# Kernel optimization log

Measured on AMD Instinct MI355X. Metric: run time of the kernel, lower is better.

The kernel has to match this reference:

```python
import jax, jax.numpy as jnp
import numpy as np

N_HEADS = 16

def setup_inputs() -> dict:
    key = jax.random.key(0)
    ks = jax.random.split(key, 6)
    B, S, D = 2, 2048, 1024
    return {
        "hidden_states": jax.random.normal(ks[0], (B, S, D), dtype=jnp.float32),
        "Wq": jax.random.normal(ks[1], (D, D), dtype=jnp.float32) * (1.0 / np.sqrt(D)),
        "Wk": jax.random.normal(ks[2], (D, D), dtype=jnp.float32) * (1.0 / np.sqrt(D)),
        "Wv": jax.random.normal(ks[3], (D, D), dtype=jnp.float32) * (1.0 / np.sqrt(D)),
        "Wo": jax.random.normal(ks[4], (D, D), dtype=jnp.float32) * (1.0 / np.sqrt(D)),
        "bo": jnp.zeros((D,), dtype=jnp.float32),
    }

def reference(hidden_states, Wq, Wk, Wv, Wo, bo):
    B, S, D = hidden_states.shape
    H = N_HEADS
    hd = D // H  # head_dim; d_kv == d_model per module's final view
    # nn.Linear(bias=False): x @ W.T, then the module's direct view to (B, H, S, hd)
    q = (hidden_states @ Wq.T).reshape(B, H, S, hd)
    k = (hidden_states @ Wk.T).reshape(B, H, S, hd)  # self-attention path (encoder_states=None)
    v = (hidden_states @ Wv.T).reshape(B, H, S, hd)
    # naive full score matrix [B, H, S, S]
    wei = jnp.einsum('bhqd,bhkd->bhqk', q, k)
    causal = jnp.tril(jnp.ones((S, S), dtype=bool))
    wei = jnp.where(causal, wei, -jnp.inf)
    # NOTE: module divides logits by head_dim (not sqrt) -- preserved faithfully
    attn = jax.nn.softmax(wei / hd, axis=-1)
    ctx = jnp.einsum('bhqk,bhkd->bhqd', attn, v)  # [B, H, S, hd]
    out = ctx.transpose(0, 2, 1, 3).reshape(B, S, D)
    return out @ Wo.T + bo
```

## Files before the change

### kernel.cpp

```cpp
#include <hip/hip_runtime.h>

#define S_LEN   2048
#define D_MODEL 1024
#define N_HEADS 16
#define HEAD_DIM 64

typedef unsigned short u16;
typedef float  floatx4 __attribute__((ext_vector_type(4)));
typedef short  bf16x8  __attribute__((ext_vector_type(8)));

__device__ __forceinline__ u16 f2bf(float f) {
    unsigned int u = __float_as_uint(f);
    u += 0x7FFF + ((u >> 16) & 1);
    return (u16)(u >> 16);
}
__device__ __forceinline__ unsigned pack2bf(float a, float b) {
    return (unsigned)f2bf(a) | ((unsigned)f2bf(b) << 16);
}

__device__ __forceinline__ void gload_lds16(const void* g, void* l) {
    __builtin_amdgcn_global_load_lds(
        reinterpret_cast<const __attribute__((address_space(1))) unsigned int*>(
            reinterpret_cast<uintptr_t>(g)),
        reinterpret_cast<__attribute__((address_space(3))) unsigned int*>(
            reinterpret_cast<uintptr_t>(l)),
        16, 0, 0);
}

__global__ __launch_bounds__(256) void cast_hs(const float* __restrict__ src,
                                               u16* __restrict__ dst) {
    const int i = (blockIdx.x * 256 + threadIdx.x) * 8;
    const float4 a = *(const float4*)(src + i);
    const float4 b = *(const float4*)(src + i + 4);
    uint4 o;
    o.x = pack2bf(a.x, a.y); o.y = pack2bf(a.z, a.w);
    o.z = pack2bf(b.x, b.y); o.w = pack2bf(b.z, b.w);
    *(uint4*)(dst + i) = o;
}

__global__ __launch_bounds__(256) void cast_w(const float* __restrict__ w0,
                                              const float* __restrict__ w1,
                                              const float* __restrict__ w2,
                                              const float* __restrict__ w3,
                                              u16* __restrict__ dst) {
    const float* srcs[4] = {w0, w1, w2, w3};
    const float* src = srcs[blockIdx.y];
    u16* o = dst + (size_t)blockIdx.y * (D_MODEL * D_MODEL);
    const int i = (blockIdx.x * 256 + threadIdx.x) * 8;
    const float4 a = *(const float4*)(src + i);
    const float4 b = *(const float4*)(src + i + 4);
    uint4 v;
    v.x = pack2bf(a.x, a.y); v.y = pack2bf(a.z, a.w);
    v.z = pack2bf(b.x, b.y); v.w = pack2bf(b.z, b.w);
    *(uint4*)(o + i) = v;
}

__global__ __launch_bounds__(256) void vtrans(const u16* __restrict__ Vf,
                                              u16* __restrict__ Vt) {
    __shared__ unsigned T[64 * 133];
    const int bh = blockIdx.y;
    const int sBase = blockIdx.x * 128;
    const u16* src = Vf + (size_t)bh * (S_LEN * HEAD_DIM) + (size_t)sBase * HEAD_DIM;
    u16* dst = Vt + (size_t)bh * (S_LEN * HEAD_DIM) + sBase;
    const int tid = threadIdx.x;

#pragma unroll
    for (int it = 0; it < 4; ++it) {
        const int idx = it * 256 + tid;
        const int row = idx >> 3, ch = idx & 7;
        const float4 v4 = *(const float4*)(src + row * 64 + ch * 8);
        const u16* vs = (const u16*)&v4;
#pragma unroll
        for (int j = 0; j < 8; ++j) T[(ch * 8 + j) * 133 + row] = vs[j];
    }
    __syncthreads();
#pragma unroll
    for (int it = 0; it < 4; ++it) {
        const int idx = it * 256 + tid;
        const int d = idx >> 4, sc = idx & 15;
        union { u16 u[8]; float4 f; } tmp;
#pragma unroll
        for (int j = 0; j < 8; ++j) tmp.u[j] = (u16)T[d * 133 + sc * 8 + j];
        *(float4*)(dst + (size_t)d * S_LEN + sc * 8) = tmp.f;
    }
}

__global__ __launch_bounds__(256) void gemm_qkv(const u16* __restrict__ A,
                                                const u16* __restrict__ Wq,
                                                const u16* __restrict__ Wk,
                                                const u16* __restrict__ Wv,
                                                u16* __restrict__ Qo,
                                                u16* __restrict__ Ko,
                                                u16* __restrict__ Vfo) {
    __shared__ u16 As[8 * 512];
    __shared__ u16 Ws[8 * 512];

    const int which = blockIdx.x >> 3;
    const int nBase = (blockIdx.x & 7) * 128;
    const int mBase = blockIdx.y * 128;
    const u16* W = which == 0 ? Wq : which == 1 ? Wk : Wv;

    const int tid = threadIdx.x, lane = tid & 63, wv = tid >> 6;
    const int l15 = lane & 15, quad = lane >> 4;
    const int wm = wv & 1, wn = wv >> 1;
    const int srow = lane >> 2;
    const int gch  = (lane & 3) ^ ((lane >> 3) & 3);
    const int swz  = (l15 >> 1) & 3;

    floatx4 acc[4][4];
#pragma unroll
    for (int i = 0; i < 4; ++i)
#pragma unroll
        for (int j = 0; j < 4; ++j) acc[i][j] = (floatx4)(0.0f);

    for (int k0 = 0; k0 < D_MODEL; k0 += 32) {
        __syncthreads();
#pragma unroll
        for (int t = 0; t < 2; ++t) {
            const int ci = wv * 2 + t;
            gload_lds16(A + (size_t)(mBase + ci * 16 + srow) * D_MODEL + k0 + gch * 8,
                        &As[ci * 512]);
            gload_lds16(W + (size_t)(nBase + ci * 16 + srow) * D_MODEL + k0 + gch * 8,
                        &Ws[ci * 512]);
        }
        __syncthreads();

        bf16x8 af[4], bfr[4];
#pragma unroll
        for (int mt = 0; mt < 4; ++mt)
            af[mt] = *(const bf16x8*)&As[(wm * 64 + mt * 16 + l15) * 32 + (quad ^ swz) * 8];
#pragma unroll
        for (int nt = 0; nt < 4; ++nt)
            bfr[nt] = *(const bf16x8*)&Ws[(wn * 64 + nt * 16 + l15) * 32 + (quad ^ swz) * 8];
#pragma unroll
        for (int mt = 0; mt < 4; ++mt)
#pragma unroll
            for (int nt = 0; nt < 4; ++nt)
                acc[mt][nt] = __builtin_amdgcn_mfma_f32_16x16x32_bf16(af[mt], bfr[nt], acc[mt][nt], 0, 0, 0);
    }

    u16* O = which == 0 ? Qo : (which == 1 ? Ko : Vfo);
    const float scale = which == 0 ? (1.44269504088896f / 64.0f) : 1.0f;
#pragma unroll
    for (int mt = 0; mt < 4; ++mt)
#pragma unroll
        for (int nt = 0; nt < 4; ++nt) {
            const int col = nBase + wn * 64 + nt * 16 + l15;
#pragma unroll
            for (int r = 0; r < 4; ++r) {
                const int row = mBase + wm * 64 + mt * 16 + quad * 4 + r;
                O[(size_t)row * D_MODEL + col] = f2bf(acc[mt][nt][r] * scale);
            }
        }
}

__global__ __launch_bounds__(256) void gemm_out(const u16* __restrict__ A,
                                                const u16* __restrict__ W,
                                                const float* __restrict__ bias,
                                                float* __restrict__ C) {
    __shared__ u16 As[8 * 512];
    __shared__ u16 Ws[8 * 512];

    const int nBase = blockIdx.x * 128;
    const int mBase = blockIdx.y * 128;
    const int tid = threadIdx.x, lane = tid & 63, wv = tid >> 6;
    const int l15 = lane & 15, quad = lane >> 4;
    const int wm = wv & 1, wn = wv >> 1;
    const int srow = lane >> 2;
    const int gch  = (lane & 3) ^ ((lane >> 3) & 3);
    const int swz  = (l15 >> 1) & 3;

    floatx4 acc[4][4];
#pragma unroll
    for (int i = 0; i < 4; ++i)
#pragma unroll
        for (int j = 0; j < 4; ++j) acc[i][j] = (floatx4)(0.0f);

    for (int k0 = 0; k0 < D_MODEL; k0 += 32) {
        __syncthreads();
#pragma unroll
        for (int t = 0; t < 2; ++t) {
            const int ci = wv * 2 + t;
            gload_lds16(A + (size_t)(mBase + ci * 16 + srow) * D_MODEL + k0 + gch * 8,
                        &As[ci * 512]);
            gload_lds16(W + (size_t)(nBase + ci * 16 + srow) * D_MODEL + k0 + gch * 8,
                        &Ws[ci * 512]);
        }
        __syncthreads();

        bf16x8 af[4], bfr[4];
#pragma unroll
        for (int mt = 0; mt < 4; ++mt)
            af[mt] = *(const bf16x8*)&As[(wm * 64 + mt * 16 + l15) * 32 + (quad ^ swz) * 8];
#pragma unroll
        for (int nt = 0; nt < 4; ++nt)
            bfr[nt] = *(const bf16x8*)&Ws[(wn * 64 + nt * 16 + l15) * 32 + (quad ^ swz) * 8];
#pragma unroll
        for (int mt = 0; mt < 4; ++mt)
#pragma unroll
            for (int nt = 0; nt < 4; ++nt)
                acc[mt][nt] = __builtin_amdgcn_mfma_f32_16x16x32_bf16(af[mt], bfr[nt], acc[mt][nt], 0, 0, 0);
    }

#pragma unroll
    for (int mt = 0; mt < 4; ++mt)
#pragma unroll
        for (int nt = 0; nt < 4; ++nt) {
            const int col = nBase + wn * 64 + nt * 16 + l15;
            const float bv = bias[col];
#pragma unroll
            for (int r = 0; r < 4; ++r) {
                const int row = mBase + wm * 64 + mt * 16 + quad * 4 + r;
                C[(size_t)row * D_MODEL + col] = acc[mt][nt][r] + bv;
            }
        }
}

__global__ __launch_bounds__(256) void attn2(const u16* __restrict__ Q,
                                             const u16* __restrict__ K,
                                             const u16* __restrict__ Vt,
                                             u16* __restrict__ Ctx) {
    __shared__ u16 Ks[8 * 512];
    __shared__ u16 Vs[8 * 512];
    __shared__ u16 Ps[4][16 * 72];

    const int pair = blockIdx.x;
    const int h = blockIdx.y, b = blockIdx.z;
    const int tid = threadIdx.x, lane = tid & 63, wv = tid >> 6;
    const int l15 = lane & 15, quad = lane >> 4;

    const size_t headOff = ((size_t)b * N_HEADS + h) * S_LEN * HEAD_DIM;
    const u16* Qh = Q + headOff;
    const u16* Kh = K + headOff;
    const u16* Vh = Vt + headOff;
    u16* Cb = Ctx + (size_t)b * S_LEN * D_MODEL + (size_t)h * HEAD_DIM;

    const int srow = lane >> 3;
    const int gch  = (lane & 7) ^ srow;
    const int swz  = l15 & 7;

    for (int half = 0; half < 2; ++half) {
        const int qt = half ? (31 - pair) : pair;
        const int qBase = qt * 64;

        bf16x8 qa[2];
#pragma unroll
        for (int ks = 0; ks < 2; ++ks)
            qa[ks] = *(const bf16x8*)(Qh + (size_t)(qBase + wv * 16 + l15) * 64 + ks * 32 + quad * 8);

        floatx4 o[4];
        float lp[4];
#pragma unroll
        for (int r = 0; r < 4; ++r) lp[r] = 0.0f;
#pragma unroll
        for (int nt = 0; nt < 4; ++nt) o[nt] = (floatx4)(0.0f);

        for (int kt = 0; kt <= qt; ++kt) {
            const int kBase = kt * 64;
            __syncthreads();
#pragma unroll
            for (int t = 0; t < 2; ++t) {
                const int ci = wv * 2 + t;
                gload_lds16(Kh + (size_t)(kBase + ci * 8 + srow) * 64 + gch * 8, &Ks[ci * 512]);
                gload_lds16(Vh + (size_t)(ci * 8 + srow) * S_LEN + kBase + gch * 8, &Vs[ci * 512]);
            }
            __syncthreads();

            floatx4 s[4];
#pragma unroll
            for (int nt = 0; nt < 4; ++nt) {
                s[nt] = (floatx4)(0.0f);
#pragma unroll
                for (int ks = 0; ks < 2; ++ks) {
                    const bf16x8 kb = *(const bf16x8*)&Ks[(nt * 16 + l15) * 64 + ((ks * 4 + quad) ^ swz) * 8];
                    s[nt] = __builtin_amdgcn_mfma_f32_16x16x32_bf16(qa[ks], kb, s[nt], 0, 0, 0);
                }
            }

            if (kt == qt) {
                const int dq = kBase + l15 - (qBase + wv * 16 + quad * 4);
#pragma unroll
                for (int nt = 0; nt < 4; ++nt)
#pragma unroll
                    for (int r = 0; r < 4; ++r) {
                        float p = exp2f(s[nt][r]);
                        p = (dq + nt * 16 > r) ? 0.0f : p;
                        lp[r] += p;
                        Ps[wv][(quad * 4 + r) * 72 + nt * 16 + l15] =
                            (u16)(__float_as_uint(p) >> 16);
                    }
            } else {
#pragma unroll
                for (int nt = 0; nt < 4; ++nt)
#pragma unroll
                    for (int r = 0; r < 4; ++r) {
                        const float p = exp2f(s[nt][r]);
                        lp[r] += p;
                        Ps[wv][(quad * 4 + r) * 72 + nt * 16 + l15] =
                            (u16)(__float_as_uint(p) >> 16);
                    }
            }

            bf16x8 pa[2];
#pragma unroll
            for (int ks = 0; ks < 2; ++ks)
                pa[ks] = *(const bf16x8*)&Ps[wv][l15 * 72 + ks * 32 + quad * 8];
#pragma unroll
            for (int nt = 0; nt < 4; ++nt)
#pragma unroll
                for (int ks = 0; ks < 2; ++ks) {
                    const bf16x8 vb = *(const bf16x8*)&Vs[(nt * 16 + l15) * 64 + ((ks * 4 + quad) ^ swz) * 8];
                    o[nt] = __builtin_amdgcn_mfma_f32_16x16x32_bf16(pa[ks], vb, o[nt], 0, 0, 0);
                }
        }

#pragma unroll
        for (int r = 0; r < 4; ++r) {
#pragma unroll
            for (int off = 1; off < 16; off <<= 1) lp[r] += __shfl_xor(lp[r], off);
            const float inv = 1.0f / lp[r];
            const int row = qBase + wv * 16 + quad * 4 + r;
#pragma unroll
            for (int nt = 0; nt < 4; ++nt)
                Cb[(size_t)row * D_MODEL + nt * 16 + l15] = f2bf(o[nt][r] * inv);
        }
    }
}

extern "C" void kernel_launch(void* const* d_in, const int* in_sizes, int n_in,
                              void* d_out, int out_size, void* d_ws, size_t ws_size,
                              hipStream_t stream) {
    const float* hs = (const float*)d_in[0];
    const float* Wq = (const float*)d_in[1];
    const float* Wk = (const float*)d_in[2];
    const float* Wv = (const float*)d_in[3];
    const float* Wo = (const float*)d_in[4];
    const float* bo = (const float*)d_in[5];
    float* out = (float*)d_out;

    const size_t NHS = (size_t)2 * S_LEN * D_MODEL;
    const size_t NW  = (size_t)D_MODEL * D_MODEL;

    u16* hsb = (u16*)d_ws;
    u16* Wb  = hsb + NHS;
    u16* Qb  = Wb + 4 * NW;
    u16* Kb  = Qb + NHS;
    u16* Vfb = Kb + NHS;
    u16* Vtb = Vfb + NHS;
    u16* Cxb = Vtb + NHS;

    cast_hs<<<2048, 256, 0, stream>>>(hs, hsb);
    cast_w<<<dim3(512, 4), 256, 0, stream>>>(Wq, Wk, Wv, Wo, Wb);

    gemm_qkv<<<dim3(24, 32), 256, 0, stream>>>(hsb, Wb, Wb + NW, Wb + 2 * NW,
                                               Qb, Kb, Vfb);

    vtrans<<<dim3(16, 32), 256, 0, stream>>>(Vfb, Vtb);

    attn2<<<dim3(16, N_HEADS, 2), 256, 0, stream>>>(Qb, Kb, Vtb, Cxb);

    gemm_out<<<dim3(8, 32), 256, 0, stream>>>(Cxb, Wb + 3 * NW, bo, out);
}
```

Baseline: 198.0 us.

## Double-buffer attention K/V loads, transpose score MFMA, merge casts, shrink out-GEMM tile

The attention kernel now double-buffers the K and V tiles in LDS, so the next tile's global-to-LDS load is issued while the current tile is being computed, and each iteration needs one barrier instead of two. It also swaps the MFMA operands so each lane holds a column of scores, which allows packed 64-bit stores of P and a single row-sum reduction, and it remaps the block index so blocks of the same head land near each other. The two cast kernels are merged into one launch, and the output GEMM uses 64-row tiles to double its grid for better occupancy across CUs. The cost is more LDS per attention block and less data reuse per output-GEMM block.

New measurement: 178.4 us. 1.11x faster.

```diff
diff --git a/kernel.cpp b/kernel.cpp
--- a/kernel.cpp
+++ b/kernel.cpp
@@ -27,32 +27,29 @@
         16, 0, 0);
 }
 
-__global__ __launch_bounds__(256) void cast_hs(const float* __restrict__ src,
-                                               u16* __restrict__ dst) {
-    const int i = (blockIdx.x * 256 + threadIdx.x) * 8;
-    const float4 a = *(const float4*)(src + i);
-    const float4 b = *(const float4*)(src + i + 4);
+__global__ __launch_bounds__(256) void cast_all(const float* __restrict__ hs,
+                                                const float* __restrict__ w0,
+                                                const float* __restrict__ w1,
+                                                const float* __restrict__ w2,
+                                                const float* __restrict__ w3,
+                                                u16* __restrict__ dst) {
+    const size_t NHS = (size_t)2 * S_LEN * D_MODEL;
+    const size_t e0 = (size_t)blockIdx.x * 2048;
+    const float* src;
+    size_t base;
+    if (e0 < NHS)                 { src = hs; base = 0; }
+    else {
+        const int wi = (int)((e0 - NHS) >> 20);
+        src = wi == 0 ? w0 : wi == 1 ? w1 : wi == 2 ? w2 : w3;
+        base = NHS + ((size_t)wi << 20);
+    }
+    const size_t i = e0 + (size_t)threadIdx.x * 8;
+    const float4 a = *(const float4*)(src + (i - base));
+    const float4 b = *(const float4*)(src + (i - base) + 4);
     uint4 o;
     o.x = pack2bf(a.x, a.y); o.y = pack2bf(a.z, a.w);
     o.z = pack2bf(b.x, b.y); o.w = pack2bf(b.z, b.w);
     *(uint4*)(dst + i) = o;
-}
-
-__global__ __launch_bounds__(256) void cast_w(const float* __restrict__ w0,
-                                              const float* __restrict__ w1,
-                                              const float* __restrict__ w2,
-                                              const float* __restrict__ w3,
-                                              u16* __restrict__ dst) {
-    const float* srcs[4] = {w0, w1, w2, w3};
-    const float* src = srcs[blockIdx.y];
-    u16* o = dst + (size_t)blockIdx.y * (D_MODEL * D_MODEL);
-    const int i = (blockIdx.x * 256 + threadIdx.x) * 8;
-    const float4 a = *(const float4*)(src + i);
-    const float4 b = *(const float4*)(src + i + 4);
-    uint4 v;
-    v.x = pack2bf(a.x, a.y); v.y = pack2bf(a.z, a.w);
-    v.z = pack2bf(b.x, b.y); v.w = pack2bf(b.z, b.w);
-    *(uint4*)(o + i) = v;
 }
 
 __global__ __launch_bounds__(256) void vtrans(const u16* __restrict__ Vf,
@@ -158,11 +155,11 @@
                                                 const u16* __restrict__ W,
                                                 const float* __restrict__ bias,
                                                 float* __restrict__ C) {
-    __shared__ u16 As[8 * 512];
+    __shared__ u16 As[4 * 512];
     __shared__ u16 Ws[8 * 512];
 
     const int nBase = blockIdx.x * 128;
-    const int mBase = blockIdx.y * 128;
+    const int mBase = blockIdx.y * 64;
     const int tid = threadIdx.x, lane = tid & 63, wv = tid >> 6;
     const int l15 = lane & 15, quad = lane >> 4;
     const int wm = wv & 1, wn = wv >> 1;
@@ -170,62 +167,65 @@
     const int gch  = (lane & 3) ^ ((lane >> 3) & 3);
     const int swz  = (l15 >> 1) & 3;
 
-    floatx4 acc[4][4];
-#pragma unroll
-    for (int i = 0; i < 4; ++i)
+    floatx4 acc[2][4];
+#pragma unroll
+    for (int i = 0; i < 2; ++i)
 #pragma unroll
         for (int j = 0; j < 4; ++j) acc[i][j] = (floatx4)(0.0f);
 
     for (int k0 = 0; k0 < D_MODEL; k0 += 32) {
         __syncthreads();
+        gload_lds16(A + (size_t)(mBase + wv * 16 + srow) * D_MODEL + k0 + gch * 8,
+                    &As[wv * 512]);
 #pragma unroll
         for (int t = 0; t < 2; ++t) {
             const int ci = wv * 2 + t;
-            gload_lds16(A + (size_t)(mBase + ci * 16 + srow) * D_MODEL + k0 + gch * 8,
-                        &As[ci * 512]);
             gload_lds16(W + (size_t)(nBase + ci * 16 + srow) * D_MODEL + k0 + gch * 8,
                         &Ws[ci * 512]);
         }
         __syncthreads();
 
-        bf16x8 af[4], bfr[4];
-#pragma unroll
-        for (int mt = 0; mt < 4; ++mt)
-            af[mt] = *(const bf16x8*)&As[(wm * 64 + mt * 16 + l15) * 32 + (quad ^ swz) * 8];
+        bf16x8 af[2], bfr[4];
+#pragma unroll
+        for (int mt = 0; mt < 2; ++mt)
+            af[mt] = *(const bf16x8*)&As[(wm * 32 + mt * 16 + l15) * 32 + (quad ^ swz) * 8];
 #pragma unroll
         for (int nt = 0; nt < 4; ++nt)
             bfr[nt] = *(const bf16x8*)&Ws[(wn * 64 + nt * 16 + l15) * 32 + (quad ^ swz) * 8];
 #pragma unroll
-        for (int mt = 0; mt < 4; ++mt)
+        for (int mt = 0; mt < 2; ++mt)
 #pragma unroll
             for (int nt = 0; nt < 4; ++nt)
                 acc[mt][nt] = __builtin_amdgcn_mfma_f32_16x16x32_bf16(af[mt], bfr[nt], acc[mt][nt], 0, 0, 0);
     }
 
 #pragma unroll
-    for (int mt = 0; mt < 4; ++mt)
+    for (int mt = 0; mt < 2; ++mt)
 #pragma unroll
         for (int nt = 0; nt < 4; ++nt) {
             const int col = nBase + wn * 64 + nt * 16 + l15;
             const float bv = bias[col];
 #pragma unroll
             for (int r = 0; r < 4; ++r) {
-                const int row = mBase + wm * 64 + mt * 16 + quad * 4 + r;
+                const int row = mBase + wm * 32 + mt * 16 + quad * 4 + r;
                 C[(size_t)row * D_MODEL + col] = acc[mt][nt][r] + bv;
             }
         }
 }
 
-__global__ __launch_bounds__(256) void attn2(const u16* __restrict__ Q,
+__global__ __launch_bounds__(256) void attn3(const u16* __restrict__ Q,
                                              const u16* __restrict__ K,
                                              const u16* __restrict__ Vt,
                                              u16* __restrict__ Ctx) {
-    __shared__ u16 Ks[8 * 512];
-    __shared__ u16 Vs[8 * 512];
+    __shared__ u16 Ks[2][8 * 512];
+    __shared__ u16 Vs[2][8 * 512];
     __shared__ u16 Ps[4][16 * 72];
 
-    const int pair = blockIdx.x;
-    const int h = blockIdx.y, b = blockIdx.z;
+    const int flat = blockIdx.x;
+    const int g    = (flat & 7) | ((flat >> 7) << 3);
+    const int pair = (flat >> 3) & 15;
+    const int h = g & 15, b = g >> 4;
+
     const int tid = threadIdx.x, lane = tid & 63, wv = tid >> 6;
     const int l15 = lane & 15, quad = lane >> 4;
 
@@ -249,56 +249,59 @@
             qa[ks] = *(const bf16x8*)(Qh + (size_t)(qBase + wv * 16 + l15) * 64 + ks * 32 + quad * 8);
 
         floatx4 o[4];
-        float lp[4];
-#pragma unroll
-        for (int r = 0; r < 4; ++r) lp[r] = 0.0f;
 #pragma unroll
         for (int nt = 0; nt < 4; ++nt) o[nt] = (floatx4)(0.0f);
-
+        float lp = 0.0f;
+
+        __syncthreads();
+#pragma unroll
+        for (int t = 0; t < 2; ++t) {
+            const int ci = wv * 2 + t;
+            gload_lds16(Kh + (size_t)(ci * 8 + srow) * 64 + gch * 8, &Ks[0][ci * 512]);
+            gload_lds16(Vh + (size_t)(ci * 8 + srow) * S_LEN + gch * 8, &Vs[0][ci * 512]);
+        }
+
+        int cur = 0;
         for (int kt = 0; kt <= qt; ++kt) {
-            const int kBase = kt * 64;
             __syncthreads();
-#pragma unroll
-            for (int t = 0; t < 2; ++t) {
-                const int ci = wv * 2 + t;
-                gload_lds16(Kh + (size_t)(kBase + ci * 8 + srow) * 64 + gch * 8, &Ks[ci * 512]);
-                gload_lds16(Vh + (size_t)(ci * 8 + srow) * S_LEN + kBase + gch * 8, &Vs[ci * 512]);
-            }
-            __syncthreads();
+            if (kt < qt) {
+                const int nb = (kt + 1) * 64;
+#pragma unroll
+                for (int t = 0; t < 2; ++t) {
+                    const int ci = wv * 2 + t;
+                    gload_lds16(Kh + (size_t)(nb + ci * 8 + srow) * 64 + gch * 8,
+                                &Ks[cur ^ 1][ci * 512]);
+                    gload_lds16(Vh + (size_t)(ci * 8 + srow) * S_LEN + nb + gch * 8,
+                                &Vs[cur ^ 1][ci * 512]);
+                }
+            }
 
             floatx4 s[4];
 #pragma unroll
-            for (int nt = 0; nt < 4; ++nt) {
-                s[nt] = (floatx4)(0.0f);
+            for (int mt = 0; mt < 4; ++mt) {
+                s[mt] = (floatx4)(0.0f);
 #pragma unroll
                 for (int ks = 0; ks < 2; ++ks) {
-                    const bf16x8 kb = *(const bf16x8*)&Ks[(nt * 16 + l15) * 64 + ((ks * 4 + quad) ^ swz) * 8];
-                    s[nt] = __builtin_amdgcn_mfma_f32_16x16x32_bf16(qa[ks], kb, s[nt], 0, 0, 0);
+                    const bf16x8 kb = *(const bf16x8*)&Ks[cur][(mt * 16 + l15) * 64 + ((ks * 4 + quad) ^ swz) * 8];
+                    s[mt] = __builtin_amdgcn_mfma_f32_16x16x32_bf16(kb, qa[ks], s[mt], 0, 0, 0);
                 }
             }
 
-            if (kt == qt) {
-                const int dq = kBase + l15 - (qBase + wv * 16 + quad * 4);
-#pragma unroll
-                for (int nt = 0; nt < 4; ++nt)
-#pragma unroll
-                    for (int r = 0; r < 4; ++r) {
-                        float p = exp2f(s[nt][r]);
-                        p = (dq + nt * 16 > r) ? 0.0f : p;
-                        lp[r] += p;
-                        Ps[wv][(quad * 4 + r) * 72 + nt * 16 + l15] =
-                            (u16)(__float_as_uint(p) >> 16);
-                    }
-            } else {
-#pragma unroll
-                for (int nt = 0; nt < 4; ++nt)
-#pragma unroll
-                    for (int r = 0; r < 4; ++r) {
-                        const float p = exp2f(s[nt][r]);
-                        lp[r] += p;
-                        Ps[wv][(quad * 4 + r) * 72 + nt * 16 + l15] =
-                            (u16)(__float_as_uint(p) >> 16);
-                    }
+            const bool diag = (kt == qt);
+#pragma unroll
+            for (int mt = 0; mt < 4; ++mt) {
+                float p[4];
+#pragma unroll
+                for (int r = 0; r < 4; ++r) {
+                    float pv = exp2f(s[mt][r]);
+                    if (diag && (mt * 16 + quad * 4 + r > wv * 16 + l15)) pv = 0.0f;
+                    p[r] = pv;
+                    lp += pv;
+                }
+                uint2 w;
+                w.x = __builtin_amdgcn_perm(__float_as_uint(p[1]), __float_as_uint(p[0]), 0x07060302);
+                w.y = __builtin_amdgcn_perm(__float_as_uint(p[3]), __float_as_uint(p[2]), 0x07060302);
+                *(uint2*)&Ps[wv][l15 * 72 + mt * 16 + quad * 4] = w;
             }
 
             bf16x8 pa[2];
@@ -309,16 +312,18 @@
             for (int nt = 0; nt < 4; ++nt)
 #pragma unroll
                 for (int ks = 0; ks < 2; ++ks) {
-                    const bf16x8 vb = *(const bf16x8*)&Vs[(nt * 16 + l15) * 64 + ((ks * 4 + quad) ^ swz) * 8];
+                    const bf16x8 vb = *(const bf16x8*)&Vs[cur][(nt * 16 + l15) * 64 + ((ks * 4 + quad) ^ swz) * 8];
                     o[nt] = __builtin_amdgcn_mfma_f32_16x16x32_bf16(pa[ks], vb, o[nt], 0, 0, 0);
                 }
-        }
+            cur ^= 1;
+        }
+
+        lp += __shfl_xor(lp, 16);
+        lp += __shfl_xor(lp, 32);
 
 #pragma unroll
         for (int r = 0; r < 4; ++r) {
-#pragma unroll
-            for (int off = 1; off < 16; off <<= 1) lp[r] += __shfl_xor(lp[r], off);
-            const float inv = 1.0f / lp[r];
+            const float inv = 1.0f / __shfl(lp, quad * 4 + r);
             const int row = qBase + wv * 16 + quad * 4 + r;
 #pragma unroll
             for (int nt = 0; nt < 4; ++nt)
@@ -349,15 +354,14 @@
     u16* Vtb = Vfb + NHS;
     u16* Cxb = Vtb + NHS;
 
-    cast_hs<<<2048, 256, 0, stream>>>(hs, hsb);
-    cast_w<<<dim3(512, 4), 256, 0, stream>>>(Wq, Wk, Wv, Wo, Wb);
+    cast_all<<<4096, 256, 0, stream>>>(hs, Wq, Wk, Wv, Wo, hsb);
 
     gemm_qkv<<<dim3(24, 32), 256, 0, stream>>>(hsb, Wb, Wb + NW, Wb + 2 * NW,
                                                Qb, Kb, Vfb);
 
     vtrans<<<dim3(16, 32), 256, 0, stream>>>(Vfb, Vtb);
 
-    attn2<<<dim3(16, N_HEADS, 2), 256, 0, stream>>>(Qb, Kb, Vtb, Cxb);
-
-    gemm_out<<<dim3(8, 32), 256, 0, stream>>>(Cxb, Wb + 3 * NW, bo, out);
-}
+    attn3<<<512, 256, 0, stream>>>(Qb, Kb, Vtb, Cxb);
+
+    gemm_out<<<dim3(8, 64), 256, 0, stream>>>(Cxb, Wb + 3 * NW, bo, out);
+}
```
